# Kernel tuning notes

Measured on AMD Instinct MI355X. Metric: run time of the kernel, lower is better.

## Reference

```python
import jax, jax.numpy as jnp
import numpy as np

K = 1024
D = 64
BETA = 0.25


def setup_inputs() -> dict:
    key = jax.random.key(0)
    k1, k2 = jax.random.split(key)
    x = jax.random.normal(k1, (32, D, 64, 64), dtype=jnp.float32)
    # torch init: uniform(-1/K, 1/K)
    emb = jax.random.uniform(k2, (K, D), dtype=jnp.float32, minval=-1.0 / K, maxval=1.0 / K)
    return {"x": x, "emb": emb}


def reference(x, emb):
    B, C, H, W = x.shape
    z = jnp.transpose(x, (0, 2, 3, 1))          # [B,H,W,D]
    zf = z.reshape(-1, C)                        # [N,D]
    # squared euclidean distances ||z||^2 + ||e||^2 - 2 z.e
    dist = (jnp.sum(zf * zf, axis=1, keepdims=True)
            + jnp.sum(emb * emb, axis=1)
            - 2.0 * jnp.matmul(zf, emb.T))       # [N,K]
    min_idx = jnp.argmin(dist, axis=1)           # [N]
    # one-hot @ emb == gather
    z_q = emb[min_idx].reshape(z.shape)          # [B,H,W,D]
    sg = jax.lax.stop_gradient
    embedding_loss = (jnp.mean((sg(z_q) - z) ** 2)
                      + BETA * jnp.mean((z_q - sg(z)) ** 2))
    z_q_st = z + sg(z_q - z)                     # straight-through
    # code-usage perplexity
    n = zf.shape[0]
    e_mean = jnp.bincount(min_idx, length=K).astype(z.dtype) / n
    perplexity = jnp.exp(-jnp.sum(e_mean * jnp.log(e_mean + 1e-10)))
    z_q_out = jnp.transpose(z_q_st, (0, 3, 1, 2))  # [B,D,H,W]
    return embedding_loss, z_q_out, perplexity
```

## Files before the change

kernel.cpp:

```cpp
#include <hip/hip_runtime.h>
#include <math.h>

#define D_    64
#define K_    1024
#define N_    131072
#define HW_   4096
#define TAU   4e-5f
#define NKT   64

typedef unsigned long long ull;
typedef unsigned short ushort;
typedef short  bf16x8  __attribute__((ext_vector_type(8)));
typedef float  f32x4   __attribute__((ext_vector_type(4)));
typedef ushort ushort8 __attribute__((ext_vector_type(8)));

__device__ __forceinline__ ushort f2bf(float f) {
    unsigned u = __float_as_uint(f);
    return (ushort)((u + 0x7FFFu + ((u >> 16) & 1u)) >> 16);
}
__device__ __forceinline__ float b2f(ushort h) {
    return __uint_as_float((unsigned)h << 16);
}

__global__ __launch_bounds__(256)
void vq_prep(const float* __restrict__ emb, ushort* __restrict__ ehg,
             ushort* __restrict__ elg, float* __restrict__ e2g,
             float* __restrict__ embT, int* __restrict__ hist,
             int* __restrict__ cnt, double* __restrict__ ssqd) {
    const int n = blockIdx.x * 256 + threadIdx.x;
    if (n < K_) {
        const float* er = emb + (size_t)n * D_;
        float e2 = 0.0f;
        #pragma unroll
        for (int d8 = 0; d8 < 8; ++d8) {
            ushort8 hh, ll;
            #pragma unroll
            for (int j = 0; j < 8; ++j) {
                float e = er[d8 * 8 + j];
                e2 = fmaf(e, e, e2);
                ushort h = f2bf(e);
                hh[j] = h;
                ll[j] = f2bf(e - b2f(h));
                embT[(size_t)(d8 * 8 + j) * K_ + n] = e;
            }
            *(ushort8*)(ehg + (size_t)n * D_ + d8 * 8) = hh;
            *(ushort8*)(elg + (size_t)n * D_ + d8 * 8) = ll;
        }
        e2g[n] = e2;
        hist[n] = 0;
    }
    if (n == 0 && blockIdx.x == 0) { *cnt = 0; *ssqd = 0.0; }
}

__global__ __launch_bounds__(256, 2)
void vq_mfma(const float* __restrict__ x, const float* __restrict__ emb,
             const ushort* __restrict__ ehg, const ushort* __restrict__ elg,
             const float* __restrict__ e2g, float* __restrict__ zq_out,
             int* __restrict__ list, int* __restrict__ cnt,
             int* __restrict__ hist, double* __restrict__ ssqd) {
    __shared__ ushort bst[2][2][8][16][8];
    __shared__ int lkfin[256];

    const int tid = threadIdx.x;
    const int wv  = tid >> 6;
    const int l   = tid & 63;
    const int g   = l >> 4;
    const int c16 = l & 15;
    const int n0b = blockIdx.x * 256;
    const int n0w = n0b + wv * 64;

    const int sHalf = tid >> 7;
    const int sS    = tid & 127;
    const int sCode = sS >> 3;
    const int sSeg  = sS & 7;
    const ushort* sBase = (sHalf ? elg : ehg) + (size_t)sCode * D_ + sSeg * 8;

    bf16x8 ah[4][2], al[4][2];
    #pragma unroll
    for (int t = 0; t < 4; ++t) {
        const int row = n0w + t * 16 + c16;
        const int b = row >> 12, hw = row & (HW_ - 1);
        const float* xr = x + (size_t)b * (D_ * HW_) + hw;
        #pragma unroll
        for (int s = 0; s < 2; ++s) {
            #pragma unroll
            for (int j = 0; j < 8; ++j) {
                float z = xr[(size_t)(g * 8 + s * 32 + j) * HW_];
                ushort h = f2bf(z);
                ah[t][s][j] = (short)h;
                al[t][s][j] = (short)f2bf(z - b2f(h));
            }
        }
    }

    float v1[16], v2[16]; int k1[16];
    #pragma unroll
    for (int st = 0; st < 16; ++st) { v1[st] = 3.4e38f; v2[st] = 3.4e38f; k1[st] = 0; }

    {
        ushort8 pf = *(const ushort8*)(sBase);
        *(ushort8*)(&bst[0][sHalf][sSeg][sCode][0]) = pf;
    }
    __syncthreads();

    for (int kt = 0; kt < NKT; ++kt) {
        const int cur = kt & 1;
        const bool more = (kt + 1) < NKT;
        ushort8 pf;
        if (more) pf = *(const ushort8*)(sBase + (size_t)(kt + 1) * 16 * D_);

        const bf16x8 bh0 = *(const bf16x8*)(&bst[cur][0][g    ][c16][0]);
        const bf16x8 bh1 = *(const bf16x8*)(&bst[cur][0][g + 4][c16][0]);
        const bf16x8 bl0 = *(const bf16x8*)(&bst[cur][1][g    ][c16][0]);
        const bf16x8 bl1 = *(const bf16x8*)(&bst[cur][1][g + 4][c16][0]);
        const int   c_  = kt * 16 + c16;
        const float E2  = e2g[c_];

        f32x4 ac[4];
        #pragma unroll
        for (int t = 0; t < 4; ++t) {
            f32x4 a = {0.0f, 0.0f, 0.0f, 0.0f};
            a = __builtin_amdgcn_mfma_f32_16x16x32_bf16(ah[t][0], bh0, a, 0, 0, 0);
            a = __builtin_amdgcn_mfma_f32_16x16x32_bf16(al[t][0], bh0, a, 0, 0, 0);
            a = __builtin_amdgcn_mfma_f32_16x16x32_bf16(ah[t][1], bh1, a, 0, 0, 0);
            a = __builtin_amdgcn_mfma_f32_16x16x32_bf16(al[t][1], bh1, a, 0, 0, 0);
            a = __builtin_amdgcn_mfma_f32_16x16x32_bf16(ah[t][0], bl0, a, 0, 0, 0);
            a = __builtin_amdgcn_mfma_f32_16x16x32_bf16(ah[t][1], bl1, a, 0, 0, 0);
            ac[t] = a;
        }
        #pragma unroll
        for (int t = 0; t < 4; ++t) {
            #pragma unroll
            for (int q = 0; q < 4; ++q) {
                float dist = fmaf(-2.0f, ac[t][q], E2);
                const int st = t * 4 + q;
                float vmax = fmaxf(dist, v1[st]);
                bool lt = dist < v1[st];
                k1[st] = lt ? c_ : k1[st];
                v1[st] = fminf(dist, v1[st]);
                v2[st] = fminf(v2[st], vmax);
            }
        }

        if (more) *(ushort8*)(&bst[cur ^ 1][sHalf][sSeg][sCode][0]) = pf;
        __syncthreads();
    }

    #pragma unroll
    for (int off = 1; off < 16; off <<= 1) {
        #pragma unroll
        for (int st = 0; st < 16; ++st) {
            float w1 = __shfl_xor(v1[st], off, 64);
            float w2 = __shfl_xor(v2[st], off, 64);
            int   wk = __shfl_xor(k1[st], off, 64);
            float lose = (w1 < v1[st]) ? v1[st] : w1;
            v2[st] = fminf(fminf(v2[st], w2), lose);
            if (w1 < v1[st]) { v1[st] = w1; k1[st] = wk; }
        }
    }

    if (c16 == 0) {
        #pragma unroll
        for (int t = 0; t < 4; ++t) {
            #pragma unroll
            for (int q = 0; q < 4; ++q) {
                const int st = t * 4 + q;
                const int rr = wv * 64 + t * 16 + 4 * g + q;
                int kk;
                if (!(v2[st] - v1[st] > TAU)) {
                    int i = atomicAdd(cnt, 1);
                    list[i] = n0b + rr;
                    kk = -1;
                } else {
                    kk = k1[st];
                    atomicAdd(&hist[kk], 1);
                }
                lkfin[rr] = kk;
            }
        }
    }
    __syncthreads();

    const int n  = n0b + tid;
    const int b2_ = n >> 12, hw2 = n & (HW_ - 1);
    const float* xr2  = x      + (size_t)b2_ * (D_ * HW_) + hw2;
    float*       outr = zq_out + (size_t)b2_ * (D_ * HW_) + hw2;
    const int kk = lkfin[tid];
    float ls = 0.0f;
    if (kk >= 0) {
        const float* er = emb + (size_t)kk * D_;
        #pragma unroll
        for (int d = 0; d < D_; ++d) {
            float zv = xr2[(size_t)d * HW_];
            float t  = er[d] - zv;
            ls = fmaf(t, t, ls);
            outr[(size_t)d * HW_] = zv + t;
        }
    }
    #pragma unroll
    for (int o = 32; o > 0; o >>= 1) ls += __shfl_down(ls, o, 64);
    if (l == 0) atomicAdd(ssqd, (double)ls);
}

__global__ __launch_bounds__(256)
void vq_exact(const float* __restrict__ x, const float* __restrict__ emb,
              const float* __restrict__ embT, const float* __restrict__ e2g,
              const int* __restrict__ list, const int* __restrict__ cnt,
              float* __restrict__ zq_out, int* __restrict__ hist,
              double* __restrict__ ssqd) {
    const int l  = threadIdx.x & 63;
    const int gw = (blockIdx.x * 256 + threadIdx.x) >> 6;
    const int nw = (gridDim.x * 256) >> 6;
    const int C  = *cnt;
    for (int i = gw; i < C; i += nw) {
        const int n = list[i];
        const int b = n >> 12, hw = n & (HW_ - 1);
        const float* xr = x + (size_t)b * (D_ * HW_) + hw;
        const float zval = xr[(size_t)l * HW_];
        float r2 = 0.0f;
        float s[16];
        #pragma unroll
        for (int j = 0; j < 16; ++j) s[j] = 0.0f;
        for (int d = 0; d < D_; ++d) {
            const float zd = __shfl(zval, d, 64);
            r2 = fmaf(zd, zd, r2);
            const float* erow = embT + (size_t)d * K_ + l * 4;
            const float4 e0 = *(const float4*)(erow);
            const float4 e1 = *(const float4*)(erow + 256);
            const float4 e2 = *(const float4*)(erow + 512);
            const float4 e3 = *(const float4*)(erow + 768);
            s[0]  = fmaf(zd, e0.x, s[0]);  s[1]  = fmaf(zd, e0.y, s[1]);
            s[2]  = fmaf(zd, e0.z, s[2]);  s[3]  = fmaf(zd, e0.w, s[3]);
            s[4]  = fmaf(zd, e1.x, s[4]);  s[5]  = fmaf(zd, e1.y, s[5]);
            s[6]  = fmaf(zd, e1.z, s[6]);  s[7]  = fmaf(zd, e1.w, s[7]);
            s[8]  = fmaf(zd, e2.x, s[8]);  s[9]  = fmaf(zd, e2.y, s[9]);
            s[10] = fmaf(zd, e2.z, s[10]); s[11] = fmaf(zd, e2.w, s[11]);
            s[12] = fmaf(zd, e3.x, s[12]); s[13] = fmaf(zd, e3.y, s[13]);
            s[14] = fmaf(zd, e3.z, s[14]); s[15] = fmaf(zd, e3.w, s[15]);
        }
        ull best = ~0ull;
        #pragma unroll
        for (int j = 0; j < 16; ++j) {
            const int k = (j >> 2) * 256 + l * 4 + (j & 3);
            float dist = fmaf(-2.0f, s[j], r2 + e2g[k]);
            ull p = ((ull)__float_as_uint(dist) << 32) | (unsigned)k;
            if (p < best) best = p;
        }
        #pragma unroll
        for (int off = 1; off < 64; off <<= 1) {
            ull q = __shfl_xor(best, off, 64);
            if (q < best) best = q;
        }
        const int k = (int)(best & 0xffffffffull);
        const float e = emb[(size_t)k * D_ + l];
        const float t = e - zval;
        float ps = t * t;
        float* outr = zq_out + (size_t)b * (D_ * HW_) + hw;
        outr[(size_t)l * HW_] = zval + t;
        #pragma unroll
        for (int off = 32; off > 0; off >>= 1) ps += __shfl_down(ps, off, 64);
        if (l == 0) {
            atomicAdd(&hist[k], 1);
            atomicAdd(ssqd, (double)ps);
        }
    }
}

__global__ __launch_bounds__(1024)
void vq_final(const int* __restrict__ hist, const double* __restrict__ ssqd,
              float* __restrict__ out_loss, float* __restrict__ out_perp) {
    __shared__ float wred[16];
    int t = threadIdx.x;
    float cnt = (float)hist[t];
    float em  = cnt / (float)N_;
    float s   = em * logf(em + 1e-10f);
    #pragma unroll
    for (int o = 32; o > 0; o >>= 1) s += __shfl_down(s, o, 64);
    if ((t & 63) == 0) wred[t >> 6] = s;
    __syncthreads();
    if (t == 0) {
        float tot = 0.0f;
        for (int w = 0; w < 16; ++w) tot += wred[w];
        *out_perp = expf(-tot);
        float mse = (float)(*ssqd / (double)((size_t)N_ * D_));
        *out_loss = mse + 0.25f * mse;
    }
}

extern "C" void kernel_launch(void* const* d_in, const int* in_sizes, int n_in,
                              void* d_out, int out_size, void* d_ws, size_t ws_size,
                              hipStream_t stream) {
    const float* x   = (const float*)d_in[0];
    const float* emb = (const float*)d_in[1];
    float* out  = (float*)d_out;
    float* loss = out;
    float* zq   = out + 1;
    float* perp = out + 1 + (size_t)N_ * D_;

    char* w = (char*)d_ws;
    int*    list = (int*)w;     w += (size_t)N_ * 4;
    ushort* ehg  = (ushort*)w;  w += (size_t)K_ * D_ * 2;
    ushort* elg  = (ushort*)w;  w += (size_t)K_ * D_ * 2;
    float*  embT = (float*)w;   w += (size_t)K_ * D_ * 4;
    float*  e2g  = (float*)w;   w += (size_t)K_ * 4;
    int*    hist = (int*)w;     w += (size_t)K_ * 4;
    int*    cnt  = (int*)w;     w += 16;
    double* ssqd = (double*)w;

    vq_prep<<<dim3(4), dim3(256), 0, stream>>>(emb, ehg, elg, e2g, embT, hist, cnt, ssqd);
    vq_mfma<<<dim3(N_ / 256), dim3(256), 0, stream>>>(x, emb, ehg, elg, e2g, zq, list, cnt, hist, ssqd);
    vq_exact<<<dim3(2048), dim3(256), 0, stream>>>(x, emb, embT, e2g, list, cnt, zq, hist, ssqd);
    vq_final<<<dim3(1), dim3(1024), 0, stream>>>(hist, ssqd, loss, perp);
}
```

Baseline: 158.3 us.

## Split codebook across wave pairs, halve rows per block, swizzle LDS codes

Each block now handles 128 rows instead of 256. Pairs of waves split the codebook in half, each covering 512 codes over 32 stages, and their top-2 results are merged through shared memory. The LDS staging layout gets an XOR swizzle to avoid bank conflicts. The launch-bounds occupancy hint rises from 2 to 4 blocks, and the gather/write epilogue splits the 64 dimensions across two thread halves. The intent is more blocks, more parallelism and fewer idle waves, at the cost of an extra merge pass and sync, and the x fragments are loaded twice per row group.

```diff
diff --git a/kernel.cpp b/kernel.cpp
--- a/kernel.cpp
+++ b/kernel.cpp
@@ -6,7 +6,7 @@
 #define N_    131072
 #define HW_   4096
 #define TAU   4e-5f
-#define NKT   64
+#define NST   32
 
 typedef unsigned long long ull;
 typedef unsigned short ushort;
@@ -21,6 +21,7 @@
 __device__ __forceinline__ float b2f(ushort h) {
     return __uint_as_float((unsigned)h << 16);
 }
+#define SLOT(seg, code) ((seg) * 16 + ((code) ^ (seg)))
 
 __global__ __launch_bounds__(256)
 void vq_prep(const float* __restrict__ emb, ushort* __restrict__ ehg,
@@ -52,28 +53,39 @@
     if (n == 0 && blockIdx.x == 0) { *cnt = 0; *ssqd = 0.0; }
 }
 
-__global__ __launch_bounds__(256, 2)
+__global__ __launch_bounds__(256, 4)
 void vq_mfma(const float* __restrict__ x, const float* __restrict__ emb,
              const ushort* __restrict__ ehg, const ushort* __restrict__ elg,
              const float* __restrict__ e2g, float* __restrict__ zq_out,
              int* __restrict__ list, int* __restrict__ cnt,
              int* __restrict__ hist, double* __restrict__ ssqd) {
-    __shared__ ushort bst[2][2][8][16][8];
-    __shared__ int lkfin[256];
+    __shared__ ushort bst[2][2][2][128][8];
+    __shared__ float lv1[4][64], lv2[4][64];
+    __shared__ int   lk1[4][64];
+    __shared__ int   lkfin[128];
 
     const int tid = threadIdx.x;
     const int wv  = tid >> 6;
+    const int rg  = wv >> 1;
+    const int kh  = wv & 1;
     const int l   = tid & 63;
     const int g   = l >> 4;
     const int c16 = l & 15;
-    const int n0b = blockIdx.x * 256;
-    const int n0w = n0b + wv * 64;
-
-    const int sHalf = tid >> 7;
-    const int sS    = tid & 127;
-    const int sCode = sS >> 3;
-    const int sSeg  = sS & 7;
-    const ushort* sBase = (sHalf ? elg : ehg) + (size_t)sCode * D_ + sSeg * 8;
+    const int n0b = blockIdx.x * 128;
+    const int n0w = n0b + rg * 64;
+
+    const int r0i   = tid;
+    const int r1i   = tid + 256;
+    const int kh0   = r0i >> 8,        kh1   = r1i >> 8;
+    const int half0 = (r0i >> 7) & 1,  half1 = (r1i >> 7) & 1;
+    const int code0 = (r0i >> 3) & 15, code1 = (r1i >> 3) & 15;
+    const int seg0  = r0i & 7,         seg1  = r1i & 7;
+    const ushort* s0Base = (half0 ? elg : ehg) + (size_t)(kh0 * NST * 16 + code0) * D_ + seg0 * 8;
+    const ushort* s1Base = (half1 ? elg : ehg) + (size_t)(kh1 * NST * 16 + code1) * D_ + seg1 * 8;
+    ushort* s0Dst[2] = { &bst[0][kh0][half0][SLOT(seg0, code0)][0],
+                         &bst[1][kh0][half0][SLOT(seg0, code0)][0] };
+    ushort* s1Dst[2] = { &bst[0][kh1][half1][SLOT(seg1, code1)][0],
+                         &bst[1][kh1][half1][SLOT(seg1, code1)][0] };
 
     bf16x8 ah[4][2], al[4][2];
     #pragma unroll
@@ -97,23 +109,24 @@
     #pragma unroll
     for (int st = 0; st < 16; ++st) { v1[st] = 3.4e38f; v2[st] = 3.4e38f; k1[st] = 0; }
 
-    {
-        ushort8 pf = *(const ushort8*)(sBase);
-        *(ushort8*)(&bst[0][sHalf][sSeg][sCode][0]) = pf;
-    }
+    *(ushort8*)(s0Dst[0]) = *(const ushort8*)(s0Base);
+    *(ushort8*)(s1Dst[0]) = *(const ushort8*)(s1Base);
     __syncthreads();
 
-    for (int kt = 0; kt < NKT; ++kt) {
-        const int cur = kt & 1;
-        const bool more = (kt + 1) < NKT;
-        ushort8 pf;
-        if (more) pf = *(const ushort8*)(sBase + (size_t)(kt + 1) * 16 * D_);
-
-        const bf16x8 bh0 = *(const bf16x8*)(&bst[cur][0][g    ][c16][0]);
-        const bf16x8 bh1 = *(const bf16x8*)(&bst[cur][0][g + 4][c16][0]);
-        const bf16x8 bl0 = *(const bf16x8*)(&bst[cur][1][g    ][c16][0]);
-        const bf16x8 bl1 = *(const bf16x8*)(&bst[cur][1][g + 4][c16][0]);
-        const int   c_  = kt * 16 + c16;
+    for (int s = 0; s < NST; ++s) {
+        const int cur = s & 1;
+        const bool more = (s + 1) < NST;
+        ushort8 pf0, pf1;
+        if (more) {
+            pf0 = *(const ushort8*)(s0Base + (size_t)(s + 1) * 16 * D_);
+            pf1 = *(const ushort8*)(s1Base + (size_t)(s + 1) * 16 * D_);
+        }
+
+        const bf16x8 bh0 = *(const bf16x8*)(&bst[cur][kh][0][SLOT(g,     c16)][0]);
+        const bf16x8 bh1 = *(const bf16x8*)(&bst[cur][kh][0][SLOT(g + 4, c16)][0]);
+        const bf16x8 bl0 = *(const bf16x8*)(&bst[cur][kh][1][SLOT(g,     c16)][0]);
+        const bf16x8 bl1 = *(const bf16x8*)(&bst[cur][kh][1][SLOT(g + 4, c16)][0]);
+        const int   c_  = (kh * NST + s) * 16 + c16;
         const float E2  = e2g[c_];
 
         f32x4 ac[4];
@@ -142,7 +155,10 @@
             }
         }
 
-        if (more) *(ushort8*)(&bst[cur ^ 1][sHalf][sSeg][sCode][0]) = pf;
+        if (more) {
+            *(ushort8*)(s0Dst[cur ^ 1]) = pf0;
+            *(ushort8*)(s1Dst[cur ^ 1]) = pf1;
+        }
         __syncthreads();
     }
 
@@ -165,34 +181,51 @@
             #pragma unroll
             for (int q = 0; q < 4; ++q) {
                 const int st = t * 4 + q;
-                const int rr = wv * 64 + t * 16 + 4 * g + q;
-                int kk;
-                if (!(v2[st] - v1[st] > TAU)) {
-                    int i = atomicAdd(cnt, 1);
-                    list[i] = n0b + rr;
-                    kk = -1;
-                } else {
-                    kk = k1[st];
-                    atomicAdd(&hist[kk], 1);
-                }
-                lkfin[rr] = kk;
+                const int rr = t * 16 + 4 * g + q;
+                lv1[wv][rr] = v1[st];
+                lv2[wv][rr] = v2[st];
+                lk1[wv][rr] = k1[st];
             }
         }
     }
     __syncthreads();
 
-    const int n  = n0b + tid;
+    if (tid < 128) {
+        const int rgm = tid >> 6, rr = tid & 63;
+        const float a1 = lv1[rgm * 2 + 0][rr], b1 = lv1[rgm * 2 + 1][rr];
+        const float a2 = lv2[rgm * 2 + 0][rr], b2 = lv2[rgm * 2 + 1][rr];
+        float v1m; int k1m;
+        if (b1 < a1) { v1m = b1; k1m = lk1[rgm * 2 + 1][rr]; }
+        else         { v1m = a1; k1m = lk1[rgm * 2 + 0][rr]; }
+        const float v2m = fminf(fmaxf(a1, b1), fminf(a2, b2));
+        int kk;
+        if (!(v2m - v1m > TAU)) {
+            int i = atomicAdd(cnt, 1);
+            list[i] = n0b + tid;
+            kk = -1;
+        } else {
+            kk = k1m;
+            atomicAdd(&hist[kk], 1);
+        }
+        lkfin[tid] = kk;
+    }
+    __syncthreads();
+
+    const int lr = tid & 127;
+    const int dh = tid >> 7;
+    const int n  = n0b + lr;
     const int b2_ = n >> 12, hw2 = n & (HW_ - 1);
     const float* xr2  = x      + (size_t)b2_ * (D_ * HW_) + hw2;
     float*       outr = zq_out + (size_t)b2_ * (D_ * HW_) + hw2;
-    const int kk = lkfin[tid];
+    const int kk = lkfin[lr];
     float ls = 0.0f;
     if (kk >= 0) {
-        const float* er = emb + (size_t)kk * D_;
-        #pragma unroll
-        for (int d = 0; d < D_; ++d) {
+        const float* er = emb + (size_t)kk * D_ + dh * 32;
+        #pragma unroll
+        for (int dd = 0; dd < 32; ++dd) {
+            const int d = dh * 32 + dd;
             float zv = xr2[(size_t)d * HW_];
-            float t  = er[d] - zv;
+            float t  = er[dd] - zv;
             ls = fmaf(t, t, ls);
             outr[(size_t)d * HW_] = zv + t;
         }
@@ -308,7 +341,7 @@
     double* ssqd = (double*)w;
 
     vq_prep<<<dim3(4), dim3(256), 0, stream>>>(emb, ehg, elg, e2g, embT, hist, cnt, ssqd);
-    vq_mfma<<<dim3(N_ / 256), dim3(256), 0, stream>>>(x, emb, ehg, elg, e2g, zq, list, cnt, hist, ssqd);
+    vq_mfma<<<dim3(N_ / 128), dim3(256), 0, stream>>>(x, emb, ehg, elg, e2g, zq, list, cnt, hist, ssqd);
     vq_exact<<<dim3(2048), dim3(256), 0, stream>>>(x, emb, embT, e2g, list, cnt, zq, hist, ssqd);
     vq_final<<<dim3(1), dim3(1024), 0, stream>>>(hist, ssqd, loss, perp);
 }
```

New measurement: 349.4 us. 2.21x slower.

## Deepen codebook prefetch, swizzle LDS slots, and use lighter LDS-only barrier

Applied to the files above, without the earlier changes.

The main MFMA loop is unrolled by two with two register prefetch buffers, so global loads of the bf16 codebook tiles are issued two steps ahead instead of one. The shared-memory staging layout is changed to an XOR-swizzled slot index to reduce bank conflicts on the 16-byte reads and writes. __syncthreads is replaced by an lgkmcnt(0) wait plus s_barrier, so the outstanding global prefetches are not drained at every barrier. This adds register pressure from the extra prefetch buffer, and correctness now relies on the custom barrier ordering the LDS writes.

```diff
diff --git a/kernel.cpp b/kernel.cpp
--- a/kernel.cpp
+++ b/kernel.cpp
@@ -20,6 +20,12 @@
 }
 __device__ __forceinline__ float b2f(ushort h) {
     return __uint_as_float((unsigned)h << 16);
+}
+#define SLOT(seg, code) ((seg) * 16 + ((code) ^ (seg)))
+
+__device__ __forceinline__ void block_sync_lds() {
+    asm volatile("s_waitcnt lgkmcnt(0)" ::: "memory");
+    __builtin_amdgcn_s_barrier();
 }
 
 __global__ __launch_bounds__(256)
@@ -52,13 +58,54 @@
     if (n == 0 && blockIdx.x == 0) { *cnt = 0; *ssqd = 0.0; }
 }
 
+#define STEP(CUR, S, PF)                                                      \
+    {                                                                         \
+        const bf16x8 bh0 = *(const bf16x8*)(&bst[CUR][0][SLOT(g,     c16)][0]); \
+        const bf16x8 bh1 = *(const bf16x8*)(&bst[CUR][0][SLOT(g + 4, c16)][0]); \
+        const bf16x8 bl0 = *(const bf16x8*)(&bst[CUR][1][SLOT(g,     c16)][0]); \
+        const bf16x8 bl1 = *(const bf16x8*)(&bst[CUR][1][SLOT(g + 4, c16)][0]); \
+        const int   c_  = (S) * 16 + c16;                                     \
+        const float E2  = e2g[c_];                                            \
+        f32x4 ac[4];                                                          \
+        _Pragma("unroll")                                                     \
+        for (int t = 0; t < 4; ++t) {                                         \
+            f32x4 a = {0.0f, 0.0f, 0.0f, 0.0f};                               \
+            a = __builtin_amdgcn_mfma_f32_16x16x32_bf16(ah[t][0], bh0, a, 0, 0, 0); \
+            a = __builtin_amdgcn_mfma_f32_16x16x32_bf16(al[t][0], bh0, a, 0, 0, 0); \
+            a = __builtin_amdgcn_mfma_f32_16x16x32_bf16(ah[t][1], bh1, a, 0, 0, 0); \
+            a = __builtin_amdgcn_mfma_f32_16x16x32_bf16(al[t][1], bh1, a, 0, 0, 0); \
+            a = __builtin_amdgcn_mfma_f32_16x16x32_bf16(ah[t][0], bl0, a, 0, 0, 0); \
+            a = __builtin_amdgcn_mfma_f32_16x16x32_bf16(ah[t][1], bl1, a, 0, 0, 0); \
+            ac[t] = a;                                                        \
+        }                                                                     \
+         \
+        _Pragma("unroll")                                                     \
+        for (int t = 0; t < 4; ++t) {                                         \
+            _Pragma("unroll")                                                 \
+            for (int q = 0; q < 4; ++q) {                                     \
+                float dist = fmaf(-2.0f, ac[t][q], E2);                       \
+                const int st = t * 4 + q;                                     \
+                float vmax = fmaxf(dist, v1[st]);                             \
+                bool lt = dist < v1[st];                                      \
+                k1[st] = lt ? c_ : k1[st];                                    \
+                v1[st] = fminf(dist, v1[st]);                                 \
+                v2[st] = fminf(v2[st], vmax);                                 \
+            }                                                                 \
+        }                                                                     \
+        if ((S) + 1 < NKT)                                                    \
+            *(ushort8*)(&bst[(CUR) ^ 1][sHalf][sSlot][0]) = PF;               \
+        if ((S) + 3 < NKT)                                                    \
+            PF = *(const ushort8*)(sBase + (size_t)((S) + 3) * 16 * D_);      \
+        block_sync_lds();                                                     \
+    }
+
 __global__ __launch_bounds__(256, 2)
 void vq_mfma(const float* __restrict__ x, const float* __restrict__ emb,
              const ushort* __restrict__ ehg, const ushort* __restrict__ elg,
              const float* __restrict__ e2g, float* __restrict__ zq_out,
              int* __restrict__ list, int* __restrict__ cnt,
              int* __restrict__ hist, double* __restrict__ ssqd) {
-    __shared__ ushort bst[2][2][8][16][8];
+    __shared__ ushort bst[2][2][128][8];
     __shared__ int lkfin[256];
 
     const int tid = threadIdx.x;
@@ -73,6 +120,7 @@
     const int sS    = tid & 127;
     const int sCode = sS >> 3;
     const int sSeg  = sS & 7;
+    const int sSlot = SLOT(sSeg, sCode);
     const ushort* sBase = (sHalf ? elg : ehg) + (size_t)sCode * D_ + sSeg * 8;
 
     bf16x8 ah[4][2], al[4][2];
@@ -97,53 +145,15 @@
     #pragma unroll
     for (int st = 0; st < 16; ++st) { v1[st] = 3.4e38f; v2[st] = 3.4e38f; k1[st] = 0; }
 
-    {
-        ushort8 pf = *(const ushort8*)(sBase);
-        *(ushort8*)(&bst[0][sHalf][sSeg][sCode][0]) = pf;
-    }
+    *(ushort8*)(&bst[0][sHalf][sSlot][0]) = *(const ushort8*)(sBase);
+    ushort8 pf0 = *(const ushort8*)(sBase + (size_t)1 * 16 * D_);
+    ushort8 pf1 = *(const ushort8*)(sBase + (size_t)2 * 16 * D_);
     __syncthreads();
 
-    for (int kt = 0; kt < NKT; ++kt) {
-        const int cur = kt & 1;
-        const bool more = (kt + 1) < NKT;
-        ushort8 pf;
-        if (more) pf = *(const ushort8*)(sBase + (size_t)(kt + 1) * 16 * D_);
-
-        const bf16x8 bh0 = *(const bf16x8*)(&bst[cur][0][g    ][c16][0]);
-        const bf16x8 bh1 = *(const bf16x8*)(&bst[cur][0][g + 4][c16][0]);
-        const bf16x8 bl0 = *(const bf16x8*)(&bst[cur][1][g    ][c16][0]);
-        const bf16x8 bl1 = *(const bf16x8*)(&bst[cur][1][g + 4][c16][0]);
-        const int   c_  = kt * 16 + c16;
-        const float E2  = e2g[c_];
-
-        f32x4 ac[4];
-        #pragma unroll
-        for (int t = 0; t < 4; ++t) {
-            f32x4 a = {0.0f, 0.0f, 0.0f, 0.0f};
-            a = __builtin_amdgcn_mfma_f32_16x16x32_bf16(ah[t][0], bh0, a, 0, 0, 0);
-            a = __builtin_amdgcn_mfma_f32_16x16x32_bf16(al[t][0], bh0, a, 0, 0, 0);
-            a = __builtin_amdgcn_mfma_f32_16x16x32_bf16(ah[t][1], bh1, a, 0, 0, 0);
-            a = __builtin_amdgcn_mfma_f32_16x16x32_bf16(al[t][1], bh1, a, 0, 0, 0);
-            a = __builtin_amdgcn_mfma_f32_16x16x32_bf16(ah[t][0], bl0, a, 0, 0, 0);
-            a = __builtin_amdgcn_mfma_f32_16x16x32_bf16(ah[t][1], bl1, a, 0, 0, 0);
-            ac[t] = a;
-        }
-        #pragma unroll
-        for (int t = 0; t < 4; ++t) {
-            #pragma unroll
-            for (int q = 0; q < 4; ++q) {
-                float dist = fmaf(-2.0f, ac[t][q], E2);
-                const int st = t * 4 + q;
-                float vmax = fmaxf(dist, v1[st]);
-                bool lt = dist < v1[st];
-                k1[st] = lt ? c_ : k1[st];
-                v1[st] = fminf(dist, v1[st]);
-                v2[st] = fminf(v2[st], vmax);
-            }
-        }
-
-        if (more) *(ushort8*)(&bst[cur ^ 1][sHalf][sSeg][sCode][0]) = pf;
-        __syncthreads();
+    #pragma unroll 1
+    for (int s = 0; s < NKT; s += 2) {
+        STEP(0, s,     pf0)
+        STEP(1, s + 1, pf1)
     }
 
     #pragma unroll
```

Measured after the change: 148.2 us. -6.4%, faster.

## Batch four codebook tiles per barrier with XOR-swizzled LDS and deeper prefetch

Applied to the files above, without the earlier changes.

The codebook staging loop now processes four 16-code tiles per iteration, so there are 16 block barriers instead of 64. Global prefetch runs two stages ahead in registers. The LDS layout uses an XOR swizzle on the code index to avoid bank conflicts on the B-fragment reads. The plain __syncthreads is replaced by an explicit lgkmcnt wait plus s_barrier. In exchange it uses four times the shared memory and more registers for the prefetch buffers, which could pressure occupancy at two blocks per CU.

```diff
diff --git a/kernel.cpp b/kernel.cpp
--- a/kernel.cpp
+++ b/kernel.cpp
@@ -6,7 +6,7 @@
 #define N_    131072
 #define HW_   4096
 #define TAU   4e-5f
-#define NKT   64
+#define NSS   16
 
 typedef unsigned long long ull;
 typedef unsigned short ushort;
@@ -20,6 +20,12 @@
 }
 __device__ __forceinline__ float b2f(ushort h) {
     return __uint_as_float((unsigned)h << 16);
+}
+#define SLOT(seg, code) ((seg) * 16 + ((code) ^ (seg)))
+
+__device__ __forceinline__ void block_sync_lds() {
+    asm volatile("s_waitcnt lgkmcnt(0)" ::: "memory");
+    __builtin_amdgcn_s_barrier();
 }
 
 __global__ __launch_bounds__(256)
@@ -58,7 +64,7 @@
              const float* __restrict__ e2g, float* __restrict__ zq_out,
              int* __restrict__ list, int* __restrict__ cnt,
              int* __restrict__ hist, double* __restrict__ ssqd) {
-    __shared__ ushort bst[2][2][8][16][8];
+    __shared__ ushort bst[2][4][2][128][8];
     __shared__ int lkfin[256];
 
     const int tid = threadIdx.x;
@@ -73,6 +79,7 @@
     const int sS    = tid & 127;
     const int sCode = sS >> 3;
     const int sSeg  = sS & 7;
+    const int sSlot = SLOT(sSeg, sCode);
     const ushort* sBase = (sHalf ? elg : ehg) + (size_t)sCode * D_ + sSeg * 8;
 
     bf16x8 ah[4][2], al[4][2];
@@ -97,53 +104,70 @@
     #pragma unroll
     for (int st = 0; st < 16; ++st) { v1[st] = 3.4e38f; v2[st] = 3.4e38f; k1[st] = 0; }
 
-    {
-        ushort8 pf = *(const ushort8*)(sBase);
-        *(ushort8*)(&bst[0][sHalf][sSeg][sCode][0]) = pf;
-    }
-    __syncthreads();
-
-    for (int kt = 0; kt < NKT; ++kt) {
-        const int cur = kt & 1;
-        const bool more = (kt + 1) < NKT;
-        ushort8 pf;
-        if (more) pf = *(const ushort8*)(sBase + (size_t)(kt + 1) * 16 * D_);
-
-        const bf16x8 bh0 = *(const bf16x8*)(&bst[cur][0][g    ][c16][0]);
-        const bf16x8 bh1 = *(const bf16x8*)(&bst[cur][0][g + 4][c16][0]);
-        const bf16x8 bl0 = *(const bf16x8*)(&bst[cur][1][g    ][c16][0]);
-        const bf16x8 bl1 = *(const bf16x8*)(&bst[cur][1][g + 4][c16][0]);
-        const int   c_  = kt * 16 + c16;
-        const float E2  = e2g[c_];
-
-        f32x4 ac[4];
-        #pragma unroll
-        for (int t = 0; t < 4; ++t) {
-            f32x4 a = {0.0f, 0.0f, 0.0f, 0.0f};
-            a = __builtin_amdgcn_mfma_f32_16x16x32_bf16(ah[t][0], bh0, a, 0, 0, 0);
-            a = __builtin_amdgcn_mfma_f32_16x16x32_bf16(al[t][0], bh0, a, 0, 0, 0);
-            a = __builtin_amdgcn_mfma_f32_16x16x32_bf16(ah[t][1], bh1, a, 0, 0, 0);
-            a = __builtin_amdgcn_mfma_f32_16x16x32_bf16(al[t][1], bh1, a, 0, 0, 0);
-            a = __builtin_amdgcn_mfma_f32_16x16x32_bf16(ah[t][0], bl0, a, 0, 0, 0);
-            a = __builtin_amdgcn_mfma_f32_16x16x32_bf16(ah[t][1], bl1, a, 0, 0, 0);
-            ac[t] = a;
-        }
-        #pragma unroll
-        for (int t = 0; t < 4; ++t) {
-            #pragma unroll
-            for (int q = 0; q < 4; ++q) {
-                float dist = fmaf(-2.0f, ac[t][q], E2);
-                const int st = t * 4 + q;
-                float vmax = fmaxf(dist, v1[st]);
-                bool lt = dist < v1[st];
-                k1[st] = lt ? c_ : k1[st];
-                v1[st] = fminf(dist, v1[st]);
-                v2[st] = fminf(v2[st], vmax);
-            }
-        }
-
-        if (more) *(ushort8*)(&bst[cur ^ 1][sHalf][sSeg][sCode][0]) = pf;
-        __syncthreads();
+    #pragma unroll
+    for (int j = 0; j < 4; ++j)
+        *(ushort8*)(&bst[0][j][sHalf][sSlot][0]) =
+            *(const ushort8*)(sBase + (size_t)j * 16 * D_);
+    ushort8 pfa = *(const ushort8*)(sBase + (size_t)4 * 16 * D_);
+    ushort8 pfb = *(const ushort8*)(sBase + (size_t)5 * 16 * D_);
+    ushort8 pfc = *(const ushort8*)(sBase + (size_t)6 * 16 * D_);
+    ushort8 pfd = *(const ushort8*)(sBase + (size_t)7 * 16 * D_);
+    block_sync_lds();
+
+    #pragma unroll 1
+    for (int ss = 0; ss < NSS; ++ss) {
+        const int cur = ss & 1;
+
+        #pragma unroll
+        for (int j = 0; j < 4; ++j) {
+            const bf16x8 bh0 = *(const bf16x8*)(&bst[cur][j][0][SLOT(g,     c16)][0]);
+            const bf16x8 bh1 = *(const bf16x8*)(&bst[cur][j][0][SLOT(g + 4, c16)][0]);
+            const bf16x8 bl0 = *(const bf16x8*)(&bst[cur][j][1][SLOT(g,     c16)][0]);
+            const bf16x8 bl1 = *(const bf16x8*)(&bst[cur][j][1][SLOT(g + 4, c16)][0]);
+            const int   c_  = (ss * 4 + j) * 16 + c16;
+            const float E2  = e2g[c_];
+
+            f32x4 ac[4];
+            #pragma unroll
+            for (int t = 0; t < 4; ++t) {
+                f32x4 a = {0.0f, 0.0f, 0.0f, 0.0f};
+                a = __builtin_amdgcn_mfma_f32_16x16x32_bf16(ah[t][0], bh0, a, 0, 0, 0);
+                a = __builtin_amdgcn_mfma_f32_16x16x32_bf16(al[t][0], bh0, a, 0, 0, 0);
+                a = __builtin_amdgcn_mfma_f32_16x16x32_bf16(ah[t][1], bh1, a, 0, 0, 0);
+                a = __builtin_amdgcn_mfma_f32_16x16x32_bf16(al[t][1], bh1, a, 0, 0, 0);
+                a = __builtin_amdgcn_mfma_f32_16x16x32_bf16(ah[t][0], bl0, a, 0, 0, 0);
+                a = __builtin_amdgcn_mfma_f32_16x16x32_bf16(ah[t][1], bl1, a, 0, 0, 0);
+                ac[t] = a;
+            }
+            #pragma unroll
+            for (int t = 0; t < 4; ++t) {
+                #pragma unroll
+                for (int q = 0; q < 4; ++q) {
+                    float dist = fmaf(-2.0f, ac[t][q], E2);
+                    const int st = t * 4 + q;
+                    float vmax = fmaxf(dist, v1[st]);
+                    bool lt = dist < v1[st];
+                    k1[st] = lt ? c_ : k1[st];
+                    v1[st] = fminf(dist, v1[st]);
+                    v2[st] = fminf(v2[st], vmax);
+                }
+            }
+        }
+
+        if (ss + 1 < NSS) {
+            *(ushort8*)(&bst[cur ^ 1][0][sHalf][sSlot][0]) = pfa;
+            *(ushort8*)(&bst[cur ^ 1][1][sHalf][sSlot][0]) = pfb;
+            *(ushort8*)(&bst[cur ^ 1][2][sHalf][sSlot][0]) = pfc;
+            *(ushort8*)(&bst[cur ^ 1][3][sHalf][sSlot][0]) = pfd;
+        }
+        if (ss + 2 < NSS) {
+            const ushort* pb = sBase + (size_t)(4 * (ss + 2)) * 16 * D_;
+            pfa = *(const ushort8*)(pb);
+            pfb = *(const ushort8*)(pb + (size_t)1 * 16 * D_);
+            pfc = *(const ushort8*)(pb + (size_t)2 * 16 * D_);
+            pfd = *(const ushort8*)(pb + (size_t)3 * 16 * D_);
+        }
+        block_sync_lds();
     }
 
     #pragma unroll
```

After: 149.5 us. 1.06x faster.
